# Optimization experiments

Hardware: AMD Instinct MI355X
Metric: run time of the kernel (lower is better)

The kernel has to match this reference:

```python
import jax, jax.numpy as jnp
import numpy as np

N, E, DIM = 50000, 1_600_000, 96
H = DIM // 3      # num_heads = dim/3 = 32
HD = 3            # head_dim = dim/num_heads = 3
SCALE = 2.0
EPS = 1e-5


def ln(x, g, b):
    mu = x.mean(-1, keepdims=True)
    var = ((x - mu) ** 2).mean(-1, keepdims=True)
    return (x - mu) * jax.lax.rsqrt(var + EPS) * g + b


def setup_inputs() -> dict:
    key = jax.random.key(0)
    ks = jax.random.split(key, 40)
    rn = lambda k, shp, s=0.05: jax.random.normal(k, shp, jnp.float32) * s
    inp = {
        'feat': jax.random.normal(ks[0], (N, DIM), jnp.float32),
        'edge': jax.random.normal(ks[1], (E, H), jnp.float32),
        'Wq': rn(ks[2], (DIM, DIM)), 'bq': jnp.zeros((DIM,), jnp.float32),
        'Wk': rn(ks[3], (DIM, DIM)), 'bk': jnp.zeros((DIM,), jnp.float32),
        'Wv': rn(ks[4], (DIM, DIM)), 'bv': jnp.zeros((DIM,), jnp.float32),
        'We': rn(ks[5], (H, H)), 'be': jnp.zeros((H,), jnp.float32),
        'Wb': rn(ks[6], (H, H)), 'bb': jnp.zeros((H,), jnp.float32),
        'Wvv': rn(ks[7], (DIM + H, DIM)), 'bvv': jnp.zeros((DIM,), jnp.float32),
        'Wf0': rn(ks[8], (H, 2 * H)), 'bf0': jnp.zeros((2 * H,), jnp.float32),
        'Wf1': rn(ks[9], (2 * H, H)), 'bf1': jnp.zeros((H,), jnp.float32),
        'Wm0': rn(ks[10], (DIM, 2 * DIM)), 'bm0': jnp.zeros((2 * DIM,), jnp.float32),
        'Wm1': rn(ks[11], (2 * DIM, DIM)), 'bm1': jnp.zeros((DIM,), jnp.float32),
        'g_n0': jnp.ones((DIM,), jnp.float32), 'b_n0': jnp.zeros((DIM,), jnp.float32),
        'g_e0': jnp.ones((H,), jnp.float32), 'b_e0': jnp.zeros((H,), jnp.float32),
        'g_e1': jnp.ones((H,), jnp.float32), 'b_e1': jnp.zeros((H,), jnp.float32),
        'g_m': jnp.ones((DIM,), jnp.float32), 'b_m': jnp.zeros((DIM,), jnp.float32),
        'w': jnp.zeros((1,), jnp.float32),
        'src': jax.random.randint(ks[12], (E,), 0, N),
        'dst': jax.random.randint(ks[13], (E,), 0, N),
    }
    return inp


def reference(feat, edge, Wq, bq, Wk, bk, Wv, bv, We, be, Wb, bb, Wvv, bvv,
              Wf0, bf0, Wf1, bf1, Wm0, bm0, Wm1, bm1,
              g_n0, b_n0, g_e0, b_e0, g_e1, b_e1, g_m, b_m, w, src, dst):
    n = feat.shape[0]
    h0 = ln(feat, g_n0, b_n0)            # [N, DIM]
    ew = ln(edge, g_e0, b_e0)            # [E, H]
    q = (h0 @ Wq + bq).reshape(n, H, HD)
    k = (h0 @ Wk + bk).reshape(n, H, HD)
    v = (h0 @ Wv + bv).reshape(n, H, HD)
    ve = (ew @ We + be)[:, :, None]       # [E, H, 1]
    B = ew @ Wb + bb                      # [E, H]
    # src_dot_dst('k','q'): (k[src] * q[dst]).sum(-1)
    score = jnp.sum(k[src] * q[dst], axis=-1) / SCALE + B   # [E, H]
    e = score + edge                       # [E, H]
    se = jnp.concatenate([v[src], ve], axis=-1)              # [E, H, 4]
    # edge_softmax: softmax over incoming edges of each dst node, per head
    m = jax.ops.segment_max(score, dst, num_segments=n)      # [N, H]
    ex = jnp.exp(score - m[dst])
    den = jax.ops.segment_sum(ex, dst, num_segments=n)
    att = (ex / den[dst])[:, :, None]                        # [E, H, 1]
    agg = jax.ops.segment_sum(att * se, dst, num_segments=n) # [N, H, 4]
    h = feat * (1.0 + w) + (agg.reshape(n, -1) @ Wvv + bvv)  # [N, DIM]
    # up_expert Mlp (pre-LN residual)
    hn = ln(h, g_m, b_m)
    h = h + (jax.nn.relu(hn @ Wm0 + bm0) @ Wm1 + bm1)
    # edge FFN residual
    en = ln(e, g_e1, b_e1)
    e = e + (jax.nn.relu(en @ Wf0 + bf0) @ Wf1 + bf1)
    return h, e
```

## Files before the change

### kernel.cpp

```cpp
#include <hip/hip_runtime.h>
#include <cstdint>
#include <cstddef>


typedef short  s16x8 __attribute__((ext_vector_type(8)));
typedef short  s16x4 __attribute__((ext_vector_type(4)));
typedef float  f32x4 __attribute__((ext_vector_type(4)));

__device__ __forceinline__ unsigned short f2b(float x) {
    union { float f; unsigned u; } v; v.f = x;
    unsigned r = v.u + 0x7FFF + ((v.u >> 16) & 1);
    return (unsigned short)(r >> 16);
}
__device__ __forceinline__ float b2f(unsigned short u) {
    union { unsigned u; float f; } v; v.u = ((unsigned)u) << 16; return v.f;
}

template<int MULTI, int LNA, int A16, int RELU, int RES>
__global__ __launch_bounds__(256) void mgemm_kernel(
    const void* __restrict__ Av, int lda,
    const float* __restrict__ B0, const float* __restrict__ B1,
    const float* __restrict__ B2, int ldb,
    const float* __restrict__ bias0, const float* __restrict__ bias1,
    const float* __restrict__ bias2,
    const float* __restrict__ lng, const float* __restrict__ lnbv,
    const float* __restrict__ resid, const float* __restrict__ wptr,
    float* __restrict__ C, int ldc, unsigned short* __restrict__ C16,
    int M, int K)
{
    __shared__ unsigned short sAL[64 * 200];
    __shared__ unsigned short sB[96 * 40];

    const int tid = threadIdx.x;
    const int m0 = blockIdx.x * 64;
    const int y  = blockIdx.y;
    const float* B = MULTI ? (y == 0 ? B0 : (y == 1 ? B1 : B2)) : B0;
    const int nbB = MULTI ? 0 : y * 96;
    const int nbC = y * 96;
    const int w = tid >> 6, l = tid & 63, fr = l & 15, kg = l >> 4;
    const int KP = K + 8;

    if (LNA) {
        const float* Af = (const float*)Av;
        const int row = 16 * w + fr;
        const int grow = m0 + row;
        float x[24];
        if (grow < M) {
            #pragma unroll
            for (int t = 0; t < 6; t++)
                *(float4*)&x[t * 4] = *(const float4*)(Af + (size_t)grow * lda + 24 * kg + t * 4);
        } else {
            #pragma unroll
            for (int t = 0; t < 24; t++) x[t] = 0.f;
        }
        float s = 0.f;
        #pragma unroll
        for (int t = 0; t < 24; t++) s += x[t];
        s += __shfl_xor(s, 16, 64); s += __shfl_xor(s, 32, 64);
        float mu = s * (1.f / 96.f);
        float v2 = 0.f;
        #pragma unroll
        for (int t = 0; t < 24; t++) { float d = x[t] - mu; v2 += d * d; }
        v2 += __shfl_xor(v2, 16, 64); v2 += __shfl_xor(v2, 32, 64);
        float rs = rsqrtf(v2 * (1.f / 96.f) + 1e-5f);
        #pragma unroll
        for (int t3 = 0; t3 < 3; t3++) {
            s16x8 yv;
            #pragma unroll
            for (int u = 0; u < 8; u++) {
                int cidx = 24 * kg + t3 * 8 + u;
                yv[u] = (short)f2b((x[t3 * 8 + u] - mu) * rs * lng[cidx] + lnbv[cidx]);
            }
            *(s16x8*)&sAL[row * KP + 24 * kg + t3 * 8] = yv;
        }
    } else {
        const int nseg = K >> 3;
        for (int idx = tid; idx < 64 * nseg; idx += 256) {
            int row = idx / nseg, k8 = (idx - row * nseg) * 8;
            int grow = m0 + row;
            s16x8 a8 = (s16x8){0, 0, 0, 0, 0, 0, 0, 0};
            if (grow < M) {
                if (A16) {
                    a8 = *(const s16x8*)((const unsigned short*)Av + (size_t)grow * lda + k8);
                } else {
                    const float* Af = (const float*)Av;
                    float4 v0 = *(const float4*)(Af + (size_t)grow * lda + k8);
                    float4 v1 = *(const float4*)(Af + (size_t)grow * lda + k8 + 4);
                    a8[0] = (short)f2b(v0.x); a8[1] = (short)f2b(v0.y);
                    a8[2] = (short)f2b(v0.z); a8[3] = (short)f2b(v0.w);
                    a8[4] = (short)f2b(v1.x); a8[5] = (short)f2b(v1.y);
                    a8[6] = (short)f2b(v1.z); a8[7] = (short)f2b(v1.w);
                }
            }
            *(s16x8*)&sAL[row * KP + k8] = a8;
        }
    }

    f32x4 acc[6];
    #pragma unroll
    for (int i = 0; i < 6; i++) acc[i] = (f32x4){0.f, 0.f, 0.f, 0.f};

    for (int kc = 0; kc < K; kc += 32) {
        #pragma unroll
        for (int r = 0; r < 3; r++) {
            int idx = tid + 256 * r;
            int k = idx / 24, n4 = (idx - k * 24) * 4;
            float4 v = *(const float4*)(B + (size_t)(kc + k) * ldb + nbB + n4);
            sB[(n4 + 0) * 40 + k] = f2b(v.x);
            sB[(n4 + 1) * 40 + k] = f2b(v.y);
            sB[(n4 + 2) * 40 + k] = f2b(v.z);
            sB[(n4 + 3) * 40 + k] = f2b(v.w);
        }
        __syncthreads();
        {
            s16x8 a = *(s16x8*)&sAL[(16 * w + fr) * KP + kc + kg * 8];
            #pragma unroll
            for (int nt = 0; nt < 6; nt++) {
                s16x8 b = *(s16x8*)&sB[(16 * nt + fr) * 40 + kg * 8];
                acc[nt] = __builtin_amdgcn_mfma_f32_16x16x32_bf16(a, b, acc[nt], 0, 0, 0);
            }
        }
        __syncthreads();
    }

    float scale = 1.f;
    if (RES) scale = wptr ? (1.f + wptr[0]) : 1.f;
    const float* biasp = MULTI ? (y == 0 ? bias0 : (y == 1 ? bias1 : bias2)) : bias0;
    const int bbase = MULTI ? 0 : nbB;

    #pragma unroll
    for (int nt = 0; nt < 6; nt++) {
        int cl = nt * 16 + fr;
        float bv = biasp[bbase + cl];
        int gcol = nbC + cl;
        #pragma unroll
        for (int r = 0; r < 4; r++) {
            int row = m0 + 16 * w + 4 * kg + r;
            if (row >= M) continue;
            float v = acc[nt][r] + bv;
            if (RELU) v = fmaxf(v, 0.f);
            if (RES) v += scale * resid[(size_t)row * ldc + gcol];
            C[(size_t)row * ldc + gcol] = v;
            if (MULTI && C16 != nullptr && y == 2)
                C16[(size_t)row * 96 + cl] = f2b(v);
        }
    }
}

__global__ __launch_bounds__(256) void count_kernel(
    const int* __restrict__ dst, int* __restrict__ cnt, int E)
{
    int i = blockIdx.x * 256 + threadIdx.x;
    if (i < E) atomicAdd(&cnt[dst[i]], 1);
}

__global__ __launch_bounds__(1024) void scan_kernel(
    const int* __restrict__ cnt, int* __restrict__ off, int* __restrict__ cur, int N)
{
    __shared__ int s[1024];
    const int tid = threadIdx.x;
    const int chunk = (N + 1023) >> 10;
    const int lo = tid * chunk;
    const int hi = min(lo + chunk, N);
    int sum = 0;
    for (int i = lo; i < hi; i++) sum += cnt[i];
    s[tid] = sum;
    __syncthreads();
    for (int d = 1; d < 1024; d <<= 1) {
        int v = (tid >= d) ? s[tid - d] : 0;
        __syncthreads();
        s[tid] += v;
        __syncthreads();
    }
    int base = (tid == 0) ? 0 : s[tid - 1];
    for (int i = lo; i < hi; i++) {
        off[i] = base; cur[i] = base;
        base += cnt[i];
    }
}

__global__ __launch_bounds__(256) void scatter_kernel(
    const int* __restrict__ dst, const int* __restrict__ src,
    int* __restrict__ cur, int* __restrict__ pos, int* __restrict__ srcs, int E)
{
    int i = blockIdx.x * 256 + threadIdx.x;
    if (i < E) {
        int p = atomicAdd(&cur[dst[i]], 1);
        pos[i] = p;
        srcs[p] = src[i];
    }
}

__global__ __launch_bounds__(256, 4) void edge_tile_kernel(
    const float* __restrict__ edge, const float* __restrict__ qkv,
    const int* __restrict__ src, const int* __restrict__ dst,
    const int* __restrict__ pos,
    const float* __restrict__ We, const float* __restrict__ be,
    const float* __restrict__ Wb, const float* __restrict__ bb,
    const float* __restrict__ Wf0, const float* __restrict__ bf0,
    const float* __restrict__ Wf1, const float* __restrict__ bf1,
    const float* __restrict__ ge0, const float* __restrict__ be0,
    const float* __restrict__ ge1, const float* __restrict__ be1,
    unsigned short* __restrict__ exve16, float* __restrict__ eout, int E)
{
    __shared__ float          sEV[64 * 36];
    __shared__ unsigned short sQK[64 * 40];
    __shared__ unsigned short sA [64 * 40];
    __shared__ unsigned short sB [64 * 40];
    __shared__ unsigned short sB2[32 * 72];
    __shared__ unsigned short sX [64 * 72];

    const int tid = threadIdx.x;
    const long long e0 = (long long)blockIdx.x * 64;
    const int w  = tid >> 6;
    const int l  = tid & 63;
    const int fr = l & 15;
    const int kg = l >> 4;

    {
        const int row = tid >> 2;
        const int j   = tid & 3;
        long long e = e0 + row;
        float q[24], k[24];
        if (e < E) {
            int dn = dst[e], sn = src[e];
            const float* qp = qkv + (size_t)dn * 288 + 24 * j;
            const float* kp = qkv + (size_t)sn * 288 + 96 + 24 * j;
            #pragma unroll
            for (int t = 0; t < 6; t++) {
                *(float4*)&q[t * 4] = *(const float4*)(qp + t * 4);
                *(float4*)&k[t * 4] = *(const float4*)(kp + t * 4);
            }
        } else {
            #pragma unroll
            for (int t = 0; t < 24; t++) { q[t] = 0.f; k[t] = 0.f; }
        }
        s16x8 qkb;
        #pragma unroll
        for (int t = 0; t < 8; t++) {
            float d = k[3*t]*q[3*t] + k[3*t+1]*q[3*t+1] + k[3*t+2]*q[3*t+2];
            qkb[t] = (short)f2b(0.5f * d);
        }
        *(s16x8*)&sQK[row * 40 + 8 * j] = qkb;
    }

    #pragma unroll
    for (int rr = 0; rr < 2; rr++) {
        int idx = tid + 256 * rr;
        int row = idx >> 3, c4 = (idx & 7) * 4;
        long long e = e0 + row;
        float4 v = make_float4(0.f, 0.f, 0.f, 0.f);
        if (e < E) v = *(const float4*)(edge + e * 32 + c4);
        *(float4*)&sEV[row * 36 + c4] = v;
    }
    {
        int k = tid >> 3, c4 = (tid & 7) * 4;
        float4 vb = *(const float4*)(Wb + k * 32 + c4);
        float4 ve = *(const float4*)(We + k * 32 + c4);
        sB[(c4 + 0) * 40 + k] = f2b(vb.x); sB[(c4 + 1) * 40 + k] = f2b(vb.y);
        sB[(c4 + 2) * 40 + k] = f2b(vb.z); sB[(c4 + 3) * 40 + k] = f2b(vb.w);
        sB[(32 + c4 + 0) * 40 + k] = f2b(ve.x); sB[(32 + c4 + 1) * 40 + k] = f2b(ve.y);
        sB[(32 + c4 + 2) * 40 + k] = f2b(ve.z); sB[(32 + c4 + 3) * 40 + k] = f2b(ve.w);
    }
    #pragma unroll
    for (int rr = 0; rr < 2; rr++) {
        int idx = tid + 256 * rr;
        int k = idx >> 3, c4 = (idx & 7) * 4;
        float4 v = *(const float4*)(Wf1 + k * 32 + c4);
        sB2[(c4 + 0) * 72 + k] = f2b(v.x); sB2[(c4 + 1) * 72 + k] = f2b(v.y);
        sB2[(c4 + 2) * 72 + k] = f2b(v.z); sB2[(c4 + 3) * 72 + k] = f2b(v.w);
    }
    __syncthreads();

    {
        const int row = 16 * w + (tid & 15);
        const int q = (tid & 63) >> 4;
        float x[8];
        *(float4*)&x[0] = *(float4*)&sEV[row * 36 + 8 * q];
        *(float4*)&x[4] = *(float4*)&sEV[row * 36 + 8 * q + 4];
        float s = x[0] + x[1] + x[2] + x[3] + x[4] + x[5] + x[6] + x[7];
        s += __shfl_xor(s, 16, 64); s += __shfl_xor(s, 32, 64);
        float mu = s * (1.f / 32.f);
        float v2 = 0.f;
        #pragma unroll
        for (int i = 0; i < 8; i++) { float d = x[i] - mu; v2 += d * d; }
        v2 += __shfl_xor(v2, 16, 64); v2 += __shfl_xor(v2, 32, 64);
        float rs = rsqrtf(v2 * (1.f / 32.f) + 1e-5f);
        float4 g1 = *(const float4*)(ge0 + 8 * q), g2 = *(const float4*)(ge0 + 8 * q + 4);
        float4 b1 = *(const float4*)(be0 + 8 * q), b2 = *(const float4*)(be0 + 8 * q + 4);
        float gg[8] = {g1.x, g1.y, g1.z, g1.w, g2.x, g2.y, g2.z, g2.w};
        float bs[8] = {b1.x, b1.y, b1.z, b1.w, b2.x, b2.y, b2.z, b2.w};
        s16x8 y;
        #pragma unroll
        for (int i = 0; i < 8; i++)
            y[i] = (short)f2b((x[i] - mu) * rs * gg[i] + bs[i]);
        *(s16x8*)&sA[row * 40 + 8 * q] = y;
    }
    __syncthreads();

    f32x4 acc[4];
    {
        s16x8 a = *(s16x8*)&sA[(16 * w + fr) * 40 + kg * 8];
        #pragma unroll
        for (int nt = 0; nt < 4; nt++) {
            s16x8 b = *(s16x8*)&sB[(16 * nt + fr) * 40 + kg * 8];
            f32x4 z = {0.f, 0.f, 0.f, 0.f};
            acc[nt] = __builtin_amdgcn_mfma_f32_16x16x32_bf16(a, b, z, 0, 0, 0);
        }
    }
    __syncthreads();

    #pragma unroll
    for (int nt = 0; nt < 2; nt++) {
        int col = nt * 16 + fr;
        float bbv = bb[col];
        #pragma unroll
        for (int r = 0; r < 4; r++) {
            int row = 16 * w + 4 * kg + r;
            float sc = acc[nt][r] + b2f(sQK[row * 40 + col]) + bbv;
            sX[row * 72 + col] = f2b(__expf(sc));
            float er = sc + sEV[row * 36 + col];
            sEV[row * 36 + col] = er;
        }
    }
    #pragma unroll
    for (int nt = 2; nt < 4; nt++) {
        int col = (nt - 2) * 16 + fr;
        float bev = be[col];
        #pragma unroll
        for (int r = 0; r < 4; r++) {
            int row = 16 * w + 4 * kg + r;
            sX[row * 72 + 32 + col] = f2b(acc[nt][r] + bev);
        }
    }
    #pragma unroll
    for (int rr = 0; rr < 2; rr++) {
        int idx = tid + 256 * rr;
        int k = idx >> 4, c4 = (idx & 15) * 4;
        float4 v = *(const float4*)(Wf0 + k * 64 + c4);
        sB[(c4 + 0) * 40 + k] = f2b(v.x); sB[(c4 + 1) * 40 + k] = f2b(v.y);
        sB[(c4 + 2) * 40 + k] = f2b(v.z); sB[(c4 + 3) * 40 + k] = f2b(v.w);
    }
    __syncthreads();

    #pragma unroll
    for (int rr = 0; rr < 2; rr++) {
        int idx = tid + 256 * rr;
        int row = idx >> 3, c8 = (idx & 7) * 8;
        long long e = e0 + row;
        if (e < E) {
            int p = pos[e];
            *(s16x8*)(exve16 + (size_t)p * 64 + c8) = *(s16x8*)&sX[row * 72 + c8];
        }
    }
    {
        const int row = 16 * w + (tid & 15);
        const int q = (tid & 63) >> 4;
        float x[8];
        *(float4*)&x[0] = *(float4*)&sEV[row * 36 + 8 * q];
        *(float4*)&x[4] = *(float4*)&sEV[row * 36 + 8 * q + 4];
        float s = x[0] + x[1] + x[2] + x[3] + x[4] + x[5] + x[6] + x[7];
        s += __shfl_xor(s, 16, 64); s += __shfl_xor(s, 32, 64);
        float mu = s * (1.f / 32.f);
        float v2 = 0.f;
        #pragma unroll
        for (int i = 0; i < 8; i++) { float d = x[i] - mu; v2 += d * d; }
        v2 += __shfl_xor(v2, 16, 64); v2 += __shfl_xor(v2, 32, 64);
        float rs = rsqrtf(v2 * (1.f / 32.f) + 1e-5f);
        float4 g1 = *(const float4*)(ge1 + 8 * q), g2 = *(const float4*)(ge1 + 8 * q + 4);
        float4 b1 = *(const float4*)(be1 + 8 * q), b2 = *(const float4*)(be1 + 8 * q + 4);
        float gg[8] = {g1.x, g1.y, g1.z, g1.w, g2.x, g2.y, g2.z, g2.w};
        float bs[8] = {b1.x, b1.y, b1.z, b1.w, b2.x, b2.y, b2.z, b2.w};
        s16x8 y;
        #pragma unroll
        for (int i = 0; i < 8; i++)
            y[i] = (short)f2b((x[i] - mu) * rs * gg[i] + bs[i]);
        *(s16x8*)&sA[row * 40 + 8 * q] = y;
    }
    __syncthreads();

    {
        s16x8 a = *(s16x8*)&sA[(16 * w + fr) * 40 + kg * 8];
        #pragma unroll
        for (int nt = 0; nt < 4; nt++) {
            s16x8 b = *(s16x8*)&sB[(16 * nt + fr) * 40 + kg * 8];
            f32x4 z = {0.f, 0.f, 0.f, 0.f};
            f32x4 a2 = __builtin_amdgcn_mfma_f32_16x16x32_bf16(a, b, z, 0, 0, 0);
            int col = nt * 16 + fr;
            float b0v = bf0[col];
            #pragma unroll
            for (int r = 0; r < 4; r++) {
                int row = 16 * w + 4 * kg + r;
                sX[row * 72 + col] = f2b(fmaxf(a2[r] + b0v, 0.f));
            }
        }
    }
    __syncthreads();

    {
        s16x8 a0 = *(s16x8*)&sX[(16 * w + fr) * 72 + kg * 8];
        s16x8 a1 = *(s16x8*)&sX[(16 * w + fr) * 72 + 32 + kg * 8];
        #pragma unroll
        for (int nt = 0; nt < 2; nt++) {
            s16x8 b0 = *(s16x8*)&sB2[(16 * nt + fr) * 72 + kg * 8];
            s16x8 b1 = *(s16x8*)&sB2[(16 * nt + fr) * 72 + 32 + kg * 8];
            f32x4 z = {0.f, 0.f, 0.f, 0.f};
            f32x4 t = __builtin_amdgcn_mfma_f32_16x16x32_bf16(a0, b0, z, 0, 0, 0);
            t = __builtin_amdgcn_mfma_f32_16x16x32_bf16(a1, b1, t, 0, 0, 0);
            int col = nt * 16 + fr;
            float bf1v = bf1[col];
            #pragma unroll
            for (int r = 0; r < 4; r++) {
                int row = 16 * w + 4 * kg + r;
                float out = t[r] + sEV[row * 36 + col] + bf1v;
                sEV[row * 36 + col] = out;
            }
        }
    }
    __syncthreads();

    #pragma unroll
    for (int rr = 0; rr < 2; rr++) {
        int idx = tid + 256 * rr;
        int row = idx >> 3, c4 = (idx & 7) * 4;
        long long e = e0 + row;
        if (e < E)
            *(float4*)(eout + e * 32 + c4) = *(float4*)&sEV[row * 36 + c4];
    }
}

__global__ __launch_bounds__(256) void gather_kernel(
    const unsigned short* __restrict__ exve16, const unsigned short* __restrict__ v16,
    const int* __restrict__ srcs, const int* __restrict__ off,
    const int* __restrict__ cnt, unsigned short* __restrict__ agg16, int N)
{
    __shared__ unsigned short sV16[4][2][2][96];
    __shared__ unsigned short sE16[4][2][2][64];
    const int wave = threadIdx.x >> 6;
    const int lane = threadIdx.x & 63;
    const int head = lane & 31;
    const int half = lane >> 5;
    int n = blockIdx.x * 4 + wave;
    if (n >= N) return;
    const int o = off[n], d = cnt[n];
    float a0 = 0.f, a1 = 0.f, a2 = 0.f, a3 = 0.f, den = 0.f;
    for (int i = half; i < d; i += 4) {
        const int i2 = i + 2;
        {
            int sn = srcs[o + i];
            const unsigned short* vr = v16 + (size_t)sn * 96;
            const unsigned short* er = exve16 + (size_t)(o + i) * 64;
            if (head < 12)
                *(s16x8*)&sV16[wave][half][0][head * 8] = *(const s16x8*)(vr + head * 8);
            else if (head >= 24)
                *(s16x8*)&sE16[wave][half][0][(head - 24) * 8] = *(const s16x8*)(er + (head - 24) * 8);
        }
        if (i2 < d) {
            int sn = srcs[o + i2];
            const unsigned short* vr = v16 + (size_t)sn * 96;
            const unsigned short* er = exve16 + (size_t)(o + i2) * 64;
            if (head < 12)
                *(s16x8*)&sV16[wave][half][1][head * 8] = *(const s16x8*)(vr + head * 8);
            else if (head >= 24)
                *(s16x8*)&sE16[wave][half][1][(head - 24) * 8] = *(const s16x8*)(er + (head - 24) * 8);
        }
        __builtin_amdgcn_wave_barrier();
        {
            float ex = b2f(sE16[wave][half][0][head]);
            float vv = b2f(sE16[wave][half][0][32 + head]);
            a0 += ex * b2f(sV16[wave][half][0][head * 3]);
            a1 += ex * b2f(sV16[wave][half][0][head * 3 + 1]);
            a2 += ex * b2f(sV16[wave][half][0][head * 3 + 2]);
            a3 += ex * vv;
            den += ex;
        }
        if (i2 < d) {
            float ex = b2f(sE16[wave][half][1][head]);
            float vv = b2f(sE16[wave][half][1][32 + head]);
            a0 += ex * b2f(sV16[wave][half][1][head * 3]);
            a1 += ex * b2f(sV16[wave][half][1][head * 3 + 1]);
            a2 += ex * b2f(sV16[wave][half][1][head * 3 + 2]);
            a3 += ex * vv;
            den += ex;
        }
        __builtin_amdgcn_wave_barrier();
    }
    a0 += __shfl_xor(a0, 32, 64);
    a1 += __shfl_xor(a1, 32, 64);
    a2 += __shfl_xor(a2, 32, 64);
    a3 += __shfl_xor(a3, 32, 64);
    den += __shfl_xor(den, 32, 64);
    if (half == 0) {
        float sc = (d > 0) ? 1.f / den : 0.f;
        s16x4 ov;
        ov[0] = (short)f2b(a0 * sc);
        ov[1] = (short)f2b(a1 * sc);
        ov[2] = (short)f2b(a2 * sc);
        ov[3] = (short)f2b(a3 * sc);
        *(s16x4*)(agg16 + (size_t)n * 128 + head * 4) = ov;
    }
}

extern "C" void kernel_launch(void* const* d_in, const int* in_sizes, int n_in,
                              void* d_out, int out_size, void* d_ws, size_t ws_size,
                              hipStream_t stream)
{
    (void)n_in; (void)out_size; (void)ws_size;
    const float* feat = (const float*)d_in[0];
    const float* edge = (const float*)d_in[1];
    const float* Wq   = (const float*)d_in[2];
    const float* bq   = (const float*)d_in[3];
    const float* Wk   = (const float*)d_in[4];
    const float* bk   = (const float*)d_in[5];
    const float* Wv   = (const float*)d_in[6];
    const float* bv   = (const float*)d_in[7];
    const float* We   = (const float*)d_in[8];
    const float* be   = (const float*)d_in[9];
    const float* Wb   = (const float*)d_in[10];
    const float* bb   = (const float*)d_in[11];
    const float* Wvv  = (const float*)d_in[12];
    const float* bvv  = (const float*)d_in[13];
    const float* Wf0  = (const float*)d_in[14];
    const float* bf0  = (const float*)d_in[15];
    const float* Wf1  = (const float*)d_in[16];
    const float* bf1  = (const float*)d_in[17];
    const float* Wm0  = (const float*)d_in[18];
    const float* bm0  = (const float*)d_in[19];
    const float* Wm1  = (const float*)d_in[20];
    const float* bm1  = (const float*)d_in[21];
    const float* g_n0 = (const float*)d_in[22];
    const float* b_n0 = (const float*)d_in[23];
    const float* g_e0 = (const float*)d_in[24];
    const float* b_e0 = (const float*)d_in[25];
    const float* g_e1 = (const float*)d_in[26];
    const float* b_e1 = (const float*)d_in[27];
    const float* g_m  = (const float*)d_in[28];
    const float* b_m  = (const float*)d_in[29];
    const float* wsc  = (const float*)d_in[30];
    const int*   src  = (const int*)d_in[31];
    const int*   dst  = (const int*)d_in[32];

    const int N = in_sizes[0] / 96;
    const int E = in_sizes[1] / 32;

    float* ws    = (float*)d_ws;
    float* qkv   = ws;
    float* hp    = qkv + (size_t)N * 288;
    unsigned short* agg16 = (unsigned short*)(hp + (size_t)N * 96);
    unsigned short* v16   = agg16 + (size_t)N * 128;
    unsigned short* exve16 = v16 + (size_t)N * 96;
    int*   pos   = (int*)(exve16 + (size_t)E * 64);
    int*   srcs  = pos + E;
    int*   cnt   = srcs + E;
    int*   offv  = cnt + N;
    int*   cur   = offv + N;
    float* tbuf  = ws;
    float* hout  = (float*)d_out;
    float* eoutp = (float*)d_out + (size_t)N * 96;

    hipMemsetAsync(cnt, 0, (size_t)N * sizeof(int), stream);

    const int mt = (N + 63) / 64;
    const int et = (E + 255) / 256;

    count_kernel<<<et, 256, 0, stream>>>(dst, cnt, E);
    scan_kernel<<<1, 1024, 0, stream>>>(cnt, offv, cur, N);
    scatter_kernel<<<et, 256, 0, stream>>>(dst, src, cur, pos, srcs, E);

    mgemm_kernel<1,1,0,0,0><<<dim3(mt, 3), 256, 0, stream>>>(
        feat, 96, Wq, Wk, Wv, 96, bq, bk, bv, g_n0, b_n0,
        nullptr, nullptr, qkv, 288, v16, N, 96);

    edge_tile_kernel<<<(E + 63) / 64, 256, 0, stream>>>(edge, qkv, src, dst, pos,
                                             We, be, Wb, bb, Wf0, bf0, Wf1, bf1,
                                             g_e0, b_e0, g_e1, b_e1,
                                             exve16, eoutp, E);

    gather_kernel<<<(N + 3) / 4, 256, 0, stream>>>(exve16, v16, srcs, offv, cnt, agg16, N);

    mgemm_kernel<0,0,1,0,1><<<dim3(mt, 1), 256, 0, stream>>>(
        agg16, 128, Wvv, Wvv, Wvv, 96, bvv, bvv, bvv, nullptr, nullptr,
        feat, wsc, hp, 96, nullptr, N, 128);
    mgemm_kernel<0,1,0,1,0><<<dim3(mt, 2), 256, 0, stream>>>(
        hp, 96, Wm0, Wm0, Wm0, 192, bm0, bm0, bm0, g_m, b_m,
        nullptr, nullptr, tbuf, 192, nullptr, N, 96);
    mgemm_kernel<0,0,0,0,1><<<dim3(mt, 1), 256, 0, stream>>>(
        tbuf, 192, Wm1, Wm1, Wm1, 96, bm1, bm1, bm1, nullptr, nullptr,
        hp, nullptr, hout, 96, nullptr, N, 192);
}
```

Baseline: 941.5 us.

## Process edges in dst-sorted order and precompute weighted messages for gather

Measured after the change: 1.114 ms. +18.3%, slower.

```diff
diff --git a/kernel.cpp b/kernel.cpp
--- a/kernel.cpp
+++ b/kernel.cpp
@@ -181,34 +181,37 @@
 
 __global__ __launch_bounds__(256) void scatter_kernel(
     const int* __restrict__ dst, const int* __restrict__ src,
-    int* __restrict__ cur, int* __restrict__ pos, int* __restrict__ srcs, int E)
+    int* __restrict__ cur, int* __restrict__ eidx,
+    int* __restrict__ srcs, int* __restrict__ dsts, int E)
 {
     int i = blockIdx.x * 256 + threadIdx.x;
     if (i < E) {
         int p = atomicAdd(&cur[dst[i]], 1);
-        pos[i] = p;
+        eidx[p] = i;
         srcs[p] = src[i];
-    }
-}
-
-__global__ __launch_bounds__(256, 4) void edge_tile_kernel(
+        dsts[p] = dst[i];
+    }
+}
+
+__global__ __launch_bounds__(256, 3) void edge_tile_kernel(
     const float* __restrict__ edge, const float* __restrict__ qkv,
-    const int* __restrict__ src, const int* __restrict__ dst,
-    const int* __restrict__ pos,
+    const int* __restrict__ eidx, const int* __restrict__ srcs,
+    const int* __restrict__ dsts,
     const float* __restrict__ We, const float* __restrict__ be,
     const float* __restrict__ Wb, const float* __restrict__ bb,
     const float* __restrict__ Wf0, const float* __restrict__ bf0,
     const float* __restrict__ Wf1, const float* __restrict__ bf1,
     const float* __restrict__ ge0, const float* __restrict__ be0,
     const float* __restrict__ ge1, const float* __restrict__ be1,
-    unsigned short* __restrict__ exve16, float* __restrict__ eout, int E)
+    unsigned short* __restrict__ exve5, float* __restrict__ eout, int E)
 {
     __shared__ float          sEV[64 * 36];
-    __shared__ unsigned short sQK[64 * 40];
+    __shared__ unsigned short sQK[64 * 44];
     __shared__ unsigned short sA [64 * 40];
     __shared__ unsigned short sB [64 * 40];
     __shared__ unsigned short sB2[32 * 72];
-    __shared__ unsigned short sX [64 * 72];
+    __shared__ unsigned short sX [64 * 76];
+    __shared__ unsigned short sV [64 * 100];
 
     const int tid = threadIdx.x;
     const long long e0 = (long long)blockIdx.x * 64;
@@ -220,10 +223,11 @@
     {
         const int row = tid >> 2;
         const int j   = tid & 3;
-        long long e = e0 + row;
+        long long s = e0 + row;
         float q[24], k[24];
-        if (e < E) {
-            int dn = dst[e], sn = src[e];
+        int sn = 0;
+        if (s < E) {
+            int dn = dsts[s]; sn = srcs[s];
             const float* qp = qkv + (size_t)dn * 288 + 24 * j;
             const float* kp = qkv + (size_t)sn * 288 + 96 + 24 * j;
             #pragma unroll
@@ -241,16 +245,33 @@
             float d = k[3*t]*q[3*t] + k[3*t+1]*q[3*t+1] + k[3*t+2]*q[3*t+2];
             qkb[t] = (short)f2b(0.5f * d);
         }
-        *(s16x8*)&sQK[row * 40 + 8 * j] = qkb;
+        *(s16x8*)&sQK[row * 44 + 8 * j] = qkb;
+        if (s < E) {
+            const float* vp = qkv + (size_t)sn * 288 + 192 + 24 * j;
+            #pragma unroll
+            for (int t = 0; t < 3; t++) {
+                float4 v0 = *(const float4*)(vp + t * 8);
+                float4 v1 = *(const float4*)(vp + t * 8 + 4);
+                s16x8 vb;
+                vb[0] = (short)f2b(v0.x); vb[1] = (short)f2b(v0.y);
+                vb[2] = (short)f2b(v0.z); vb[3] = (short)f2b(v0.w);
+                vb[4] = (short)f2b(v1.x); vb[5] = (short)f2b(v1.y);
+                vb[6] = (short)f2b(v1.z); vb[7] = (short)f2b(v1.w);
+                *(s16x8*)&sV[row * 100 + 24 * j + 8 * t] = vb;
+            }
+        }
     }
 
     #pragma unroll
     for (int rr = 0; rr < 2; rr++) {
         int idx = tid + 256 * rr;
         int row = idx >> 3, c4 = (idx & 7) * 4;
-        long long e = e0 + row;
+        long long s = e0 + row;
         float4 v = make_float4(0.f, 0.f, 0.f, 0.f);
-        if (e < E) v = *(const float4*)(edge + e * 32 + c4);
+        if (s < E) {
+            int ge = eidx[s];
+            v = *(const float4*)(edge + (size_t)ge * 32 + c4);
+        }
         *(float4*)&sEV[row * 36 + c4] = v;
     }
     {
@@ -317,8 +338,8 @@
         #pragma unroll
         for (int r = 0; r < 4; r++) {
             int row = 16 * w + 4 * kg + r;
-            float sc = acc[nt][r] + b2f(sQK[row * 40 + col]) + bbv;
-            sX[row * 72 + col] = f2b(__expf(sc));
+            float sc = acc[nt][r] + b2f(sQK[row * 44 + col]) + bbv;
+            sX[row * 76 + col] = f2b(__expf(sc));
             float er = sc + sEV[row * 36 + col];
             sEV[row * 36 + col] = er;
         }
@@ -330,7 +351,7 @@
         #pragma unroll
         for (int r = 0; r < 4; r++) {
             int row = 16 * w + 4 * kg + r;
-            sX[row * 72 + 32 + col] = f2b(acc[nt][r] + bev);
+            sX[row * 76 + 32 + col] = f2b(acc[nt][r] + bev);
         }
     }
     #pragma unroll
@@ -343,14 +364,40 @@
     }
     __syncthreads();
 
-    #pragma unroll
-    for (int rr = 0; rr < 2; rr++) {
-        int idx = tid + 256 * rr;
-        int row = idx >> 3, c8 = (idx & 7) * 8;
-        long long e = e0 + row;
-        if (e < E) {
-            int p = pos[e];
-            *(s16x8*)(exve16 + (size_t)p * 64 + c8) = *(s16x8*)&sX[row * 72 + c8];
+    {
+        const int row = tid >> 2;
+        const int j   = tid & 3;
+        long long s = e0 + row;
+        if (s < E) {
+            unsigned short* base = exve5 + (size_t)s * 160;
+            if (j == 0) {
+                #pragma unroll
+                for (int t = 0; t < 4; t++)
+                    *(s16x8*)(base + 8 * t) = *(s16x8*)&sX[row * 76 + 8 * t];
+            } else if (j == 3) {
+                #pragma unroll
+                for (int t = 0; t < 4; t++) {
+                    s16x8 o;
+                    #pragma unroll
+                    for (int u = 0; u < 8; u++) {
+                        int h = 8 * t + u;
+                        o[u] = (short)f2b(b2f(sX[row * 76 + h]) * b2f(sX[row * 76 + 32 + h]));
+                    }
+                    *(s16x8*)(base + 128 + 8 * t) = o;
+                }
+            } else {
+                const int m0 = (j - 1) * 48;
+                #pragma unroll
+                for (int t = 0; t < 6; t++) {
+                    s16x8 o;
+                    #pragma unroll
+                    for (int u = 0; u < 8; u++) {
+                        int m = m0 + 8 * t + u;
+                        o[u] = (short)f2b(b2f(sX[row * 76 + m / 3]) * b2f(sV[row * 100 + m]));
+                    }
+                    *(s16x8*)(base + 32 + m0 + 8 * t) = o;
+                }
+            }
         }
     }
     {
@@ -391,15 +438,15 @@
             #pragma unroll
             for (int r = 0; r < 4; r++) {
                 int row = 16 * w + 4 * kg + r;
-                sX[row * 72 + col] = f2b(fmaxf(a2[r] + b0v, 0.f));
-            }
-        }
-    }
-    __syncthreads();
-
-    {
-        s16x8 a0 = *(s16x8*)&sX[(16 * w + fr) * 72 + kg * 8];
-        s16x8 a1 = *(s16x8*)&sX[(16 * w + fr) * 72 + 32 + kg * 8];
+                sX[row * 76 + col] = f2b(fmaxf(a2[r] + b0v, 0.f));
+            }
+        }
+    }
+    __syncthreads();
+
+    {
+        s16x8 a0 = *(s16x8*)&sX[(16 * w + fr) * 76 + kg * 8];
+        s16x8 a1 = *(s16x8*)&sX[(16 * w + fr) * 76 + 32 + kg * 8];
         #pragma unroll
         for (int nt = 0; nt < 2; nt++) {
             s16x8 b0 = *(s16x8*)&sB2[(16 * nt + fr) * 72 + kg * 8];
@@ -423,81 +470,53 @@
     for (int rr = 0; rr < 2; rr++) {
         int idx = tid + 256 * rr;
         int row = idx >> 3, c4 = (idx & 7) * 4;
-        long long e = e0 + row;
-        if (e < E)
-            *(float4*)(eout + e * 32 + c4) = *(float4*)&sEV[row * 36 + c4];
+        long long s = e0 + row;
+        if (s < E) {
+            int ge = eidx[s];
+            *(float4*)(eout + (size_t)ge * 32 + c4) = *(float4*)&sEV[row * 36 + c4];
+        }
     }
 }
 
 __global__ __launch_bounds__(256) void gather_kernel(
-    const unsigned short* __restrict__ exve16, const unsigned short* __restrict__ v16,
-    const int* __restrict__ srcs, const int* __restrict__ off,
-    const int* __restrict__ cnt, unsigned short* __restrict__ agg16, int N)
+    const unsigned short* __restrict__ exve5,
+    const int* __restrict__ off, const int* __restrict__ cnt,
+    unsigned short* __restrict__ agg16, int N)
 {
-    __shared__ unsigned short sV16[4][2][2][96];
-    __shared__ unsigned short sE16[4][2][2][64];
+    __shared__ float red[4][176];
     const int wave = threadIdx.x >> 6;
     const int lane = threadIdx.x & 63;
-    const int head = lane & 31;
-    const int half = lane >> 5;
     int n = blockIdx.x * 4 + wave;
     if (n >= N) return;
     const int o = off[n], d = cnt[n];
-    float a0 = 0.f, a1 = 0.f, a2 = 0.f, a3 = 0.f, den = 0.f;
-    for (int i = half; i < d; i += 4) {
-        const int i2 = i + 2;
-        {
-            int sn = srcs[o + i];
-            const unsigned short* vr = v16 + (size_t)sn * 96;
-            const unsigned short* er = exve16 + (size_t)(o + i) * 64;
-            if (head < 12)
-                *(s16x8*)&sV16[wave][half][0][head * 8] = *(const s16x8*)(vr + head * 8);
-            else if (head >= 24)
-                *(s16x8*)&sE16[wave][half][0][(head - 24) * 8] = *(const s16x8*)(er + (head - 24) * 8);
-        }
-        if (i2 < d) {
-            int sn = srcs[o + i2];
-            const unsigned short* vr = v16 + (size_t)sn * 96;
-            const unsigned short* er = exve16 + (size_t)(o + i2) * 64;
-            if (head < 12)
-                *(s16x8*)&sV16[wave][half][1][head * 8] = *(const s16x8*)(vr + head * 8);
-            else if (head >= 24)
-                *(s16x8*)&sE16[wave][half][1][(head - 24) * 8] = *(const s16x8*)(er + (head - 24) * 8);
-        }
-        __builtin_amdgcn_wave_barrier();
-        {
-            float ex = b2f(sE16[wave][half][0][head]);
-            float vv = b2f(sE16[wave][half][0][32 + head]);
-            a0 += ex * b2f(sV16[wave][half][0][head * 3]);
-            a1 += ex * b2f(sV16[wave][half][0][head * 3 + 1]);
-            a2 += ex * b2f(sV16[wave][half][0][head * 3 + 2]);
-            a3 += ex * vv;
-            den += ex;
-        }
-        if (i2 < d) {
-            float ex = b2f(sE16[wave][half][1][head]);
-            float vv = b2f(sE16[wave][half][1][32 + head]);
-            a0 += ex * b2f(sV16[wave][half][1][head * 3]);
-            a1 += ex * b2f(sV16[wave][half][1][head * 3 + 1]);
-            a2 += ex * b2f(sV16[wave][half][1][head * 3 + 2]);
-            a3 += ex * vv;
-            den += ex;
-        }
-        __builtin_amdgcn_wave_barrier();
-    }
-    a0 += __shfl_xor(a0, 32, 64);
-    a1 += __shfl_xor(a1, 32, 64);
-    a2 += __shfl_xor(a2, 32, 64);
-    a3 += __shfl_xor(a3, 32, 64);
-    den += __shfl_xor(den, 32, 64);
-    if (half == 0) {
-        float sc = (d > 0) ? 1.f / den : 0.f;
+    const unsigned* base = (const unsigned*)exve5 + (size_t)o * 80;
+    float s0 = 0.f, s1 = 0.f, s2 = 0.f, s3 = 0.f;
+    for (int i = 0; i < d; i++) {
+        unsigned wv = base[(size_t)i * 80 + lane];
+        s0 += b2f((unsigned short)(wv & 0xFFFFu));
+        s1 += b2f((unsigned short)(wv >> 16));
+        if (lane < 16) {
+            unsigned w2 = base[(size_t)i * 80 + 64 + lane];
+            s2 += b2f((unsigned short)(w2 & 0xFFFFu));
+            s3 += b2f((unsigned short)(w2 >> 16));
+        }
+    }
+    red[wave][2 * lane]     = s0;
+    red[wave][2 * lane + 1] = s1;
+    if (lane < 16) {
+        red[wave][128 + 2 * lane] = s2;
+        red[wave][129 + 2 * lane] = s3;
+    }
+    __builtin_amdgcn_wave_barrier();
+    if (lane < 32) {
+        float den = red[wave][lane];
+        float r = (d > 0 && den != 0.f) ? 1.f / den : 0.f;
         s16x4 ov;
-        ov[0] = (short)f2b(a0 * sc);
-        ov[1] = (short)f2b(a1 * sc);
-        ov[2] = (short)f2b(a2 * sc);
-        ov[3] = (short)f2b(a3 * sc);
-        *(s16x4*)(agg16 + (size_t)n * 128 + head * 4) = ov;
+        ov[0] = (short)f2b(red[wave][32 + 3 * lane] * r);
+        ov[1] = (short)f2b(red[wave][33 + 3 * lane] * r);
+        ov[2] = (short)f2b(red[wave][34 + 3 * lane] * r);
+        ov[3] = (short)f2b(red[wave][128 + lane] * r);
+        *(s16x4*)(agg16 + (size_t)n * 128 + lane * 4) = ov;
     }
 }
 
@@ -547,11 +566,11 @@
     float* qkv   = ws;
     float* hp    = qkv + (size_t)N * 288;
     unsigned short* agg16 = (unsigned short*)(hp + (size_t)N * 96);
-    unsigned short* v16   = agg16 + (size_t)N * 128;
-    unsigned short* exve16 = v16 + (size_t)N * 96;
-    int*   pos   = (int*)(exve16 + (size_t)E * 64);
-    int*   srcs  = pos + E;
-    int*   cnt   = srcs + E;
+    unsigned short* exve5 = agg16 + (size_t)N * 128;
+    int*   eidx  = (int*)(exve5 + (size_t)E * 160);
+    int*   srcs  = eidx + E;
+    int*   dsts  = srcs + E;
+    int*   cnt   = dsts + E;
     int*   offv  = cnt + N;
     int*   cur   = offv + N;
     float* tbuf  = ws;
@@ -565,18 +584,18 @@
 
     count_kernel<<<et, 256, 0, stream>>>(dst, cnt, E);
     scan_kernel<<<1, 1024, 0, stream>>>(cnt, offv, cur, N);
-    scatter_kernel<<<et, 256, 0, stream>>>(dst, src, cur, pos, srcs, E);
+    scatter_kernel<<<et, 256, 0, stream>>>(dst, src, cur, eidx, srcs, dsts, E);
 
     mgemm_kernel<1,1,0,0,0><<<dim3(mt, 3), 256, 0, stream>>>(
         feat, 96, Wq, Wk, Wv, 96, bq, bk, bv, g_n0, b_n0,
-        nullptr, nullptr, qkv, 288, v16, N, 96);
-
-    edge_tile_kernel<<<(E + 63) / 64, 256, 0, stream>>>(edge, qkv, src, dst, pos,
+        nullptr, nullptr, qkv, 288, nullptr, N, 96);
+
+    edge_tile_kernel<<<(E + 63) / 64, 256, 0, stream>>>(edge, qkv, eidx, srcs, dsts,
                                              We, be, Wb, bb, Wf0, bf0, Wf1, bf1,
                                              g_e0, b_e0, g_e1, b_e1,
-                                             exve16, eoutp, E);
-
-    gather_kernel<<<(N + 3) / 4, 256, 0, stream>>>(exve16, v16, srcs, offv, cnt, agg16, N);
+                                             exve5, eoutp, E);
+
+    gather_kernel<<<(N + 3) / 4, 256, 0, stream>>>(exve5, offv, cnt, agg16, N);
 
     mgemm_kernel<0,0,1,0,1><<<dim3(mt, 1), 256, 0, stream>>>(
         agg16, 128, Wvv, Wvv, Wvv, 96, bvv, bvv, bvv, nullptr, nullptr,
```

## Process edges in dst-sorted order in edge tile kernel

Applied to the files above, without the earlier changes.

Measured after the change: 915.1 us. 2.8% less time.

```diff
diff --git a/kernel.cpp b/kernel.cpp
--- a/kernel.cpp
+++ b/kernel.cpp
@@ -181,20 +181,22 @@
 
 __global__ __launch_bounds__(256) void scatter_kernel(
     const int* __restrict__ dst, const int* __restrict__ src,
-    int* __restrict__ cur, int* __restrict__ pos, int* __restrict__ srcs, int E)
+    int* __restrict__ cur, int* __restrict__ eidx,
+    int* __restrict__ srcs, int* __restrict__ dsts, int E)
 {
     int i = blockIdx.x * 256 + threadIdx.x;
     if (i < E) {
         int p = atomicAdd(&cur[dst[i]], 1);
-        pos[i] = p;
+        eidx[p] = i;
         srcs[p] = src[i];
+        dsts[p] = dst[i];
     }
 }
 
 __global__ __launch_bounds__(256, 4) void edge_tile_kernel(
     const float* __restrict__ edge, const float* __restrict__ qkv,
-    const int* __restrict__ src, const int* __restrict__ dst,
-    const int* __restrict__ pos,
+    const int* __restrict__ eidx, const int* __restrict__ srcs,
+    const int* __restrict__ dsts,
     const float* __restrict__ We, const float* __restrict__ be,
     const float* __restrict__ Wb, const float* __restrict__ bb,
     const float* __restrict__ Wf0, const float* __restrict__ bf0,
@@ -204,11 +206,11 @@
     unsigned short* __restrict__ exve16, float* __restrict__ eout, int E)
 {
     __shared__ float          sEV[64 * 36];
-    __shared__ unsigned short sQK[64 * 40];
+    __shared__ unsigned short sQK[64 * 44];
     __shared__ unsigned short sA [64 * 40];
     __shared__ unsigned short sB [64 * 40];
     __shared__ unsigned short sB2[32 * 72];
-    __shared__ unsigned short sX [64 * 72];
+    __shared__ unsigned short sX [64 * 76];
 
     const int tid = threadIdx.x;
     const long long e0 = (long long)blockIdx.x * 64;
@@ -220,10 +222,10 @@
     {
         const int row = tid >> 2;
         const int j   = tid & 3;
-        long long e = e0 + row;
+        long long s = e0 + row;
         float q[24], k[24];
-        if (e < E) {
-            int dn = dst[e], sn = src[e];
+        if (s < E) {
+            int dn = dsts[s], sn = srcs[s];
             const float* qp = qkv + (size_t)dn * 288 + 24 * j;
             const float* kp = qkv + (size_t)sn * 288 + 96 + 24 * j;
             #pragma unroll
@@ -241,16 +243,19 @@
             float d = k[3*t]*q[3*t] + k[3*t+1]*q[3*t+1] + k[3*t+2]*q[3*t+2];
             qkb[t] = (short)f2b(0.5f * d);
         }
-        *(s16x8*)&sQK[row * 40 + 8 * j] = qkb;
+        *(s16x8*)&sQK[row * 44 + 8 * j] = qkb;
     }
 
     #pragma unroll
     for (int rr = 0; rr < 2; rr++) {
         int idx = tid + 256 * rr;
         int row = idx >> 3, c4 = (idx & 7) * 4;
-        long long e = e0 + row;
+        long long s = e0 + row;
         float4 v = make_float4(0.f, 0.f, 0.f, 0.f);
-        if (e < E) v = *(const float4*)(edge + e * 32 + c4);
+        if (s < E) {
+            int ge = eidx[s];
+            v = *(const float4*)(edge + (size_t)ge * 32 + c4);
+        }
         *(float4*)&sEV[row * 36 + c4] = v;
     }
     {
@@ -317,8 +322,8 @@
         #pragma unroll
         for (int r = 0; r < 4; r++) {
             int row = 16 * w + 4 * kg + r;
-            float sc = acc[nt][r] + b2f(sQK[row * 40 + col]) + bbv;
-            sX[row * 72 + col] = f2b(__expf(sc));
+            float sc = acc[nt][r] + b2f(sQK[row * 44 + col]) + bbv;
+            sX[row * 76 + col] = f2b(__expf(sc));
             float er = sc + sEV[row * 36 + col];
             sEV[row * 36 + col] = er;
         }
@@ -330,7 +335,7 @@
         #pragma unroll
         for (int r = 0; r < 4; r++) {
             int row = 16 * w + 4 * kg + r;
-            sX[row * 72 + 32 + col] = f2b(acc[nt][r] + bev);
+            sX[row * 76 + 32 + col] = f2b(acc[nt][r] + bev);
         }
     }
     #pragma unroll
@@ -347,11 +352,9 @@
     for (int rr = 0; rr < 2; rr++) {
         int idx = tid + 256 * rr;
         int row = idx >> 3, c8 = (idx & 7) * 8;
-        long long e = e0 + row;
-        if (e < E) {
-            int p = pos[e];
-            *(s16x8*)(exve16 + (size_t)p * 64 + c8) = *(s16x8*)&sX[row * 72 + c8];
-        }
+        long long s = e0 + row;
+        if (s < E)
+            *(s16x8*)(exve16 + (size_t)s * 64 + c8) = *(s16x8*)&sX[row * 76 + c8];
     }
     {
         const int row = 16 * w + (tid & 15);
@@ -391,15 +394,15 @@
             #pragma unroll
             for (int r = 0; r < 4; r++) {
                 int row = 16 * w + 4 * kg + r;
-                sX[row * 72 + col] = f2b(fmaxf(a2[r] + b0v, 0.f));
+                sX[row * 76 + col] = f2b(fmaxf(a2[r] + b0v, 0.f));
             }
         }
     }
     __syncthreads();
 
     {
-        s16x8 a0 = *(s16x8*)&sX[(16 * w + fr) * 72 + kg * 8];
-        s16x8 a1 = *(s16x8*)&sX[(16 * w + fr) * 72 + 32 + kg * 8];
+        s16x8 a0 = *(s16x8*)&sX[(16 * w + fr) * 76 + kg * 8];
+        s16x8 a1 = *(s16x8*)&sX[(16 * w + fr) * 76 + 32 + kg * 8];
         #pragma unroll
         for (int nt = 0; nt < 2; nt++) {
             s16x8 b0 = *(s16x8*)&sB2[(16 * nt + fr) * 72 + kg * 8];
@@ -423,9 +426,11 @@
     for (int rr = 0; rr < 2; rr++) {
         int idx = tid + 256 * rr;
         int row = idx >> 3, c4 = (idx & 7) * 4;
-        long long e = e0 + row;
-        if (e < E)
-            *(float4*)(eout + e * 32 + c4) = *(float4*)&sEV[row * 36 + c4];
+        long long s = e0 + row;
+        if (s < E) {
+            int ge = eidx[s];
+            *(float4*)(eout + (size_t)ge * 32 + c4) = *(float4*)&sEV[row * 36 + c4];
+        }
     }
 }
 
@@ -549,9 +554,10 @@
     unsigned short* agg16 = (unsigned short*)(hp + (size_t)N * 96);
     unsigned short* v16   = agg16 + (size_t)N * 128;
     unsigned short* exve16 = v16 + (size_t)N * 96;
-    int*   pos   = (int*)(exve16 + (size_t)E * 64);
-    int*   srcs  = pos + E;
-    int*   cnt   = srcs + E;
+    int*   eidx  = (int*)(exve16 + (size_t)E * 64);
+    int*   srcs  = eidx + E;
+    int*   dsts  = srcs + E;
+    int*   cnt   = dsts + E;
     int*   offv  = cnt + N;
     int*   cur   = offv + N;
     float* tbuf  = ws;
@@ -565,13 +571,13 @@
 
     count_kernel<<<et, 256, 0, stream>>>(dst, cnt, E);
     scan_kernel<<<1, 1024, 0, stream>>>(cnt, offv, cur, N);
-    scatter_kernel<<<et, 256, 0, stream>>>(dst, src, cur, pos, srcs, E);
+    scatter_kernel<<<et, 256, 0, stream>>>(dst, src, cur, eidx, srcs, dsts, E);
 
     mgemm_kernel<1,1,0,0,0><<<dim3(mt, 3), 256, 0, stream>>>(
         feat, 96, Wq, Wk, Wv, 96, bq, bk, bv, g_n0, b_n0,
         nullptr, nullptr, qkv, 288, v16, N, 96);
 
-    edge_tile_kernel<<<(E + 63) / 64, 256, 0, stream>>>(edge, qkv, src, dst, pos,
+    edge_tile_kernel<<<(E + 63) / 64, 256, 0, stream>>>(edge, qkv, eidx, srcs, dsts,
                                              We, be, Wb, bb, Wf0, bf0, Wf1, bf1,
                                              g_e0, b_e0, g_e1, b_e1,
                                              exve16, eoutp, E);
```
